# Kernel optimization log

Measured on AMD Instinct MI355X. Metric: run time of the kernel, lower is better.

## Reference

```python
import jax, jax.numpy as jnp
import numpy as np

B, C, H, W, D = 1, 128, 64, 64, 64
CQ = C // 8


def setup_inputs() -> dict:
    key = jax.random.key(0)
    ks = jax.random.split(key, 6)
    s = 0.05
    return {
        "x": jax.random.normal(ks[0], (B, C, H, W, D), jnp.float32),
        "y": jax.random.normal(ks[1], (B, C, H, W, D), jnp.float32),
        "Wq": jax.random.normal(ks[2], (CQ, C), jnp.float32) * s,
        "bq": jnp.zeros((CQ,), jnp.float32),
        "Wk": jax.random.normal(ks[3], (CQ, C), jnp.float32) * s,
        "bk": jnp.zeros((CQ,), jnp.float32),
        "Wv": jax.random.normal(ks[4], (C, C), jnp.float32) * s,
        "bv": jnp.zeros((C,), jnp.float32),
        # torch inits gamma to 0 (kills all attention grads); use a nonzero value
        "gamma": jax.random.normal(ks[5], (1,), jnp.float32),
    }


def _conv1x1(x, Wt, b):
    # 1x1x1 Conv3d == per-voxel linear over channels
    return jnp.einsum('bchwd,oc->bohwd', x, Wt) + b[None, :, None, None, None]


def _criss_cross(x, y, Wq, bq, Wk, bk, Wv, bv, gamma):
    Bs, Cs, Hs, Ws, Ds = x.shape
    Cq = Wq.shape[0]
    q = _conv1x1(x, Wq, bq)  # [B,Cq,H,W,D]
    k = _conv1x1(y, Wk, bk)  # [B,Cq,H,W,D]
    v = _conv1x1(x, Wv, bv)  # [B,C ,H,W,D]

    # exact transliteration of the torch permute/contiguous/view sequence
    qH = q.transpose(0, 3, 4, 1, 2).reshape(Bs * Ws * Ds, Cq, Hs).transpose(0, 2, 1)
    qW = q.transpose(0, 2, 4, 1, 3).reshape(Bs * Hs * Ds, Cq, Ws).transpose(0, 2, 1)
    qD = q.transpose(0, 2, 3, 1, 4).reshape(Bs * Hs * Ws, Cq, Ds).transpose(0, 2, 1)
    kH = k.transpose(0, 3, 4, 1, 2).reshape(Bs * Ws * Ds, Cq, Hs)
    kW = k.transpose(0, 2, 4, 1, 3).reshape(Bs * Hs * Ds, Cq, Ws)
    kD = k.transpose(0, 2, 3, 1, 4).reshape(Bs * Hs * Ws, Cq, Ds)
    vH = v.transpose(0, 3, 4, 1, 2).reshape(Bs * Ws * Ds, Cs, Hs)
    vW = v.transpose(0, 2, 4, 1, 3).reshape(Bs * Hs * Ds, Cs, Ws)
    vD = v.transpose(0, 2, 3, 1, 4).reshape(Bs * Hs * Ws, Cs, Ds)

    # INF(): -inf on the HxH diagonal, broadcast over the B*W*D batch
    inf_mask = jnp.where(jnp.eye(Hs, dtype=bool), -jnp.inf, 0.0)[None].astype(x.dtype)

    energy_H = (jnp.matmul(qH, kH) + inf_mask).reshape(Bs, Ws, Hs, Ds, Hs).transpose(0, 2, 1, 3, 4)
    energy_W = jnp.matmul(qW, kW).reshape(Bs, Hs, Ws, Ds, Ws)
    energy_D = jnp.matmul(qD, kD).reshape(Bs, Hs, Ws, Ds, Ds)

    # NOTE: original uses Softmax(dim=3) on the 5D concat -> softmax over the D axis
    concate = jax.nn.softmax(jnp.concatenate([energy_H, energy_W, energy_D], axis=4), axis=3)

    att_H = concate[..., 0:Hs].transpose(0, 2, 1, 3, 4).reshape(Bs * Ws * Ds, Hs, Hs)
    att_W = concate[..., Hs:Hs + Ws].reshape(Bs * Hs * Ds, Ws, Ws)
    att_D = concate[..., Hs + Ws:Hs + Ws + Ds].reshape(Bs * Hs * Ws, Ds, Ds)

    out_H = jnp.matmul(vH, att_H.transpose(0, 2, 1)).reshape(Bs, Ws, Cs, Hs, Ds).transpose(0, 2, 3, 1, 4)
    out_W = jnp.matmul(vW, att_W.transpose(0, 2, 1)).reshape(Bs, Hs, Cs, Ws, Ds).transpose(0, 2, 1, 3, 4)
    out_D = jnp.matmul(vD, att_D.transpose(0, 2, 1)).reshape(Bs, Hs, Cs, Ws, Ds).transpose(0, 2, 1, 3, 4)

    return gamma[0] * (out_H + out_W + out_D) + x


def reference(x, y, Wq, bq, Wk, bk, Wv, bv, gamma):
    return _criss_cross(x, y, Wq, bq, Wk, bk, Wv, bv, gamma)
```

## Files before the change

### kernel.cpp

```cpp
#include <hip/hip_runtime.h>

#define HWD 262144
#define WD  4096

typedef unsigned short bf16_t;
typedef unsigned short u16;
struct __align__(8) us4 { unsigned short x, y, z, w; };

typedef __bf16 bf16x8 __attribute__((ext_vector_type(8)));
typedef float  f32x4  __attribute__((ext_vector_type(4)));

__device__ inline float b2f(unsigned short u) {
    return __uint_as_float(((unsigned int)u) << 16);
}
__device__ inline unsigned short f2b(float f) {
    unsigned int u = __float_as_uint(f);
    u += 0x7fff + ((u >> 16) & 1);
    return (unsigned short)(u >> 16);
}

union FragU { us4 h[2]; bf16x8 v; };
__device__ inline bf16x8 ld8_a8(const u16* p) {
    FragU f; f.h[0] = *(const us4*)p; f.h[1] = *(const us4*)(p + 4); return f.v;
}
__device__ inline bf16x8 ld8_a16(const u16* p) {
    return *(const bf16x8*)p;
}

struct HL { bf16x8 h, l; };
__device__ inline HL split8(const float* w8) {
    FragU H, L;
    unsigned short hh[8], ll[8];
#pragma unroll
    for (int t = 0; t < 8; ++t) {
        hh[t] = f2b(w8[t]);
        ll[t] = f2b(w8[t] - b2f(hh[t]));
    }
    H.h[0].x = hh[0]; H.h[0].y = hh[1]; H.h[0].z = hh[2]; H.h[0].w = hh[3];
    H.h[1].x = hh[4]; H.h[1].y = hh[5]; H.h[1].z = hh[6]; H.h[1].w = hh[7];
    L.h[0].x = ll[0]; L.h[0].y = ll[1]; L.h[0].z = ll[2]; L.h[0].w = ll[3];
    L.h[1].x = ll[4]; L.h[1].y = ll[5]; L.h[1].z = ll[6]; L.h[1].w = ll[7];
    HL r; r.h = H.v; r.l = L.v; return r;
}

__global__ void prep_w_kernel(
    const float* __restrict__ Wv, const float* __restrict__ Wq,
    const float* __restrict__ Wk,
    u16* __restrict__ WSv, u16* __restrict__ WSq, u16* __restrict__ WSk)
{
    const int t = threadIdx.x;
    const float* W; u16* D; int m, ks;
    if (t < 512)      { W = Wv; D = WSv; m = t >> 2;          ks = t & 3; }
    else if (t < 576) { W = Wq; D = WSq; m = (t - 512) >> 2;  ks = t & 3; }
    else if (t < 640) { W = Wk; D = WSk; m = (t - 576) >> 2;  ks = t & 3; }
    else return;
#pragma unroll
    for (int j = 0; j < 32; ++j) {
        const float w = W[m * 128 + ks * 32 + j];
        const u16 h = f2b(w);
        const u16 l = f2b(w - b2f(h));
        D[((m * 4 + ks) * 2 + 0) * 32 + j] = h;
        D[((m * 4 + ks) * 2 + 1) * 32 + j] = l;
    }
}

__global__ __launch_bounds__(512, 4) void conv_x_mfma(
    const float* __restrict__ x, const u16* __restrict__ WSv,
    const u16* __restrict__ WSq,
    const float* __restrict__ bv, const float* __restrict__ bq,
    bf16_t* __restrict__ v, bf16_t* __restrict__ q)
{
    __shared__ __align__(16) u16 Xh[64][136];
    __shared__ __align__(16) u16 Xl[64][136];
    const int tid  = threadIdx.x;
    const int lane = tid & 63;
    const int wv   = tid >> 6;
    const int lg = lane >> 4, lr = lane & 15;
    const int n0 = blockIdx.x * 64;
    const int m0 = wv * 16;

    float v8[2][8];
#pragma unroll
    for (int gi = 0; gi < 2; ++gi) {
        const int g = wv + gi * 8;
#pragma unroll
        for (int s = 0; s < 8; ++s)
            v8[gi][s] = x[(size_t)(g * 8 + s) * HWD + n0 + lane];
    }

    bf16x8 Ah[4], Al[4], Qh[4], Ql[4];
#pragma unroll
    for (int ks = 0; ks < 4; ++ks) {
        Ah[ks] = ld8_a16(&WSv[(((m0 + lr) * 4 + ks) * 2 + 0) * 32 + lg * 8]);
        Al[ks] = ld8_a16(&WSv[(((m0 + lr) * 4 + ks) * 2 + 1) * 32 + lg * 8]);
    }
    if (wv < 4) {
#pragma unroll
        for (int ks = 0; ks < 4; ++ks) {
            Qh[ks] = ld8_a16(&WSq[((lr * 4 + ks) * 2 + 0) * 32 + lg * 8]);
            Ql[ks] = ld8_a16(&WSq[((lr * 4 + ks) * 2 + 1) * 32 + lg * 8]);
        }
    }

#pragma unroll
    for (int gi = 0; gi < 2; ++gi) {
        const int g = wv + gi * 8;
        HL hl = split8(v8[gi]);
        *(bf16x8*)&Xh[lane][g * 8] = hl.h;
        *(bf16x8*)&Xl[lane][g * 8] = hl.l;
    }
    __syncthreads();

    f32x4 acc[4];
#pragma unroll
    for (int ns = 0; ns < 4; ++ns) acc[ns] = (f32x4){0.f, 0.f, 0.f, 0.f};
    f32x4 accq = (f32x4){0.f, 0.f, 0.f, 0.f};
#pragma unroll
    for (int ks = 0; ks < 4; ++ks) {
#pragma unroll
        for (int ns = 0; ns < 4; ++ns) {
            const bf16x8 Bh = ld8_a16(&Xh[ns * 16 + lr][ks * 32 + lg * 8]);
            const bf16x8 Bl = ld8_a16(&Xl[ns * 16 + lr][ks * 32 + lg * 8]);
            acc[ns] = __builtin_amdgcn_mfma_f32_16x16x32_bf16(Ah[ks], Bh, acc[ns], 0, 0, 0);
            acc[ns] = __builtin_amdgcn_mfma_f32_16x16x32_bf16(Ah[ks], Bl, acc[ns], 0, 0, 0);
            acc[ns] = __builtin_amdgcn_mfma_f32_16x16x32_bf16(Al[ks], Bh, acc[ns], 0, 0, 0);
            if (wv < 4 && ns == wv) {
                accq = __builtin_amdgcn_mfma_f32_16x16x32_bf16(Qh[ks], Bh, accq, 0, 0, 0);
                accq = __builtin_amdgcn_mfma_f32_16x16x32_bf16(Qh[ks], Bl, accq, 0, 0, 0);
                accq = __builtin_amdgcn_mfma_f32_16x16x32_bf16(Ql[ks], Bh, accq, 0, 0, 0);
            }
        }
    }
#pragma unroll
    for (int ns = 0; ns < 4; ++ns)
#pragma unroll
        for (int r = 0; r < 4; ++r) {
            const int m = m0 + 4 * lg + r;
            v[(size_t)m * HWD + n0 + ns * 16 + lr] = f2b(acc[ns][r] + bv[m]);
        }
    if (wv < 4) {
#pragma unroll
        for (int r = 0; r < 4; ++r) {
            const int m = 4 * lg + r;
            q[(size_t)m * HWD + n0 + wv * 16 + lr] = f2b(accq[r] + bq[m]);
        }
    }
}

__global__ __launch_bounds__(256, 4) void conv_y_mfma(
    const float* __restrict__ y, const u16* __restrict__ WSk,
    const float* __restrict__ bk, bf16_t* __restrict__ k)
{
    __shared__ __align__(16) u16 Yh[64][136];
    __shared__ __align__(16) u16 Yl[64][136];
    const int tid  = threadIdx.x;
    const int lane = tid & 63;
    const int wv   = tid >> 6;
    const int lg = lane >> 4, lr = lane & 15;
    const int n0 = blockIdx.x * 64;
    const int n  = tid & 63;

    float v8[4][8];
#pragma unroll
    for (int gi = 0; gi < 4; ++gi) {
        const int g = (tid >> 6) * 4 + gi;
#pragma unroll
        for (int s = 0; s < 8; ++s)
            v8[gi][s] = y[(size_t)(g * 8 + s) * HWD + n0 + n];
    }

    bf16x8 Ah[4], Al[4];
#pragma unroll
    for (int ks = 0; ks < 4; ++ks) {
        Ah[ks] = ld8_a16(&WSk[((lr * 4 + ks) * 2 + 0) * 32 + lg * 8]);
        Al[ks] = ld8_a16(&WSk[((lr * 4 + ks) * 2 + 1) * 32 + lg * 8]);
    }

#pragma unroll
    for (int gi = 0; gi < 4; ++gi) {
        const int g = (tid >> 6) * 4 + gi;
        HL hl = split8(v8[gi]);
        *(bf16x8*)&Yh[n][g * 8] = hl.h;
        *(bf16x8*)&Yl[n][g * 8] = hl.l;
    }
    __syncthreads();

    f32x4 acc = (f32x4){0.f, 0.f, 0.f, 0.f};
#pragma unroll
    for (int ks = 0; ks < 4; ++ks) {
        const bf16x8 Bh = ld8_a16(&Yh[wv * 16 + lr][ks * 32 + lg * 8]);
        const bf16x8 Bl = ld8_a16(&Yl[wv * 16 + lr][ks * 32 + lg * 8]);
        acc = __builtin_amdgcn_mfma_f32_16x16x32_bf16(Ah[ks], Bh, acc, 0, 0, 0);
        acc = __builtin_amdgcn_mfma_f32_16x16x32_bf16(Ah[ks], Bl, acc, 0, 0, 0);
        acc = __builtin_amdgcn_mfma_f32_16x16x32_bf16(Al[ks], Bh, acc, 0, 0, 0);
    }
#pragma unroll
    for (int r = 0; r < 4; ++r) {
        const int m = 4 * lg + r;
        k[(size_t)m * HWD + n0 + wv * 16 + lr] = f2b(acc[r] + bk[m]);
    }
}

__global__ __launch_bounds__(256) void t_wd_kernel(
    const bf16_t* __restrict__ src, bf16_t* __restrict__ dst)
{
    const int h = blockIdx.x, c = blockIdx.y;
    __shared__ bf16_t tile[64][72];
    const size_t base = (size_t)c * HWD + h * WD;
    const int tid = threadIdx.x;
#pragma unroll
    for (int i = 0; i < 4; ++i) {
        const int f = (tid + i * 256) * 4;
        const int w = f >> 6, d = f & 63;
        const us4 val = *(const us4*)&src[base + w * 64 + d];
        tile[w][d] = val.x; tile[w][d + 1] = val.y;
        tile[w][d + 2] = val.z; tile[w][d + 3] = val.w;
    }
    __syncthreads();
#pragma unroll
    for (int i = 0; i < 4; ++i) {
        const int f = (tid + i * 256) * 4;
        const int d = f >> 6, w0 = f & 63;
        us4 o; o.x = tile[w0][d]; o.y = tile[w0 + 1][d];
        o.z = tile[w0 + 2][d]; o.w = tile[w0 + 3][d];
        *(us4*)&dst[base + d * 64 + w0] = o;
    }
}

__global__ __launch_bounds__(256) void t_hd_kernel(
    const bf16_t* __restrict__ src, bf16_t* __restrict__ dst)
{
    const int w = blockIdx.x, c = blockIdx.y;
    __shared__ bf16_t tile[64][72];
    const size_t cb = (size_t)c * HWD;
    const int tid = threadIdx.x;
#pragma unroll
    for (int i = 0; i < 4; ++i) {
        const int f = (tid + i * 256) * 4;
        const int h = f >> 6, d0 = f & 63;
        const us4 val = *(const us4*)&src[cb + h * WD + w * 64 + d0];
        tile[h][d0] = val.x; tile[h][d0 + 1] = val.y;
        tile[h][d0 + 2] = val.z; tile[h][d0 + 3] = val.w;
    }
    __syncthreads();
#pragma unroll
    for (int i = 0; i < 4; ++i) {
        const int f = (tid + i * 256) * 4;
        const int d = f >> 6, h0 = f & 63;
        us4 o; o.x = tile[h0][d]; o.y = tile[h0 + 1][d];
        o.z = tile[h0 + 2][d]; o.w = tile[h0 + 3][d];
        *(us4*)&dst[cb + w * WD + d * 64 + h0] = o;
    }
}

template<bool MASK>
__device__ __forceinline__ void cc_phase(
    const u16* __restrict__ qp, const u16* __restrict__ kp,
    const u16* __restrict__ vp, const size_t base, const int tid,
    u16 (*Qt)[36], u16 (*Kt)[36], u16 (*Vs)[72], u16 (*PB)[72], f32x4* acc)
{
    const int w  = tid >> 6;
    const int l  = tid & 63;
    const int lg = l >> 4, lr = l & 15;

    __syncthreads();
    const int c0 = (tid >> 6) * 4;
    const size_t gb = base + (tid & 63);
    us4 qv, kv;
    qv.x = qp[(size_t)(c0 + 0) * HWD + gb];
    qv.y = qp[(size_t)(c0 + 1) * HWD + gb];
    qv.z = qp[(size_t)(c0 + 2) * HWD + gb];
    qv.w = qp[(size_t)(c0 + 3) * HWD + gb];
    kv.x = kp[(size_t)(c0 + 0) * HWD + gb];
    kv.y = kp[(size_t)(c0 + 1) * HWD + gb];
    kv.z = kp[(size_t)(c0 + 2) * HWD + gb];
    kv.w = kp[(size_t)(c0 + 3) * HWD + gb];
    us4 vreg[8];
#pragma unroll
    for (int i = 0; i < 8; ++i) {
        const int f = (tid + i * 256) * 4;
        vreg[i] = *(const us4*)&vp[(size_t)(f >> 6) * HWD + base + (f & 63)];
    }
    {
        const int j = tid & 63;
        *(us4*)&Qt[j][c0] = qv;
        *(us4*)&Kt[j][c0] = kv;
        us4 z; z.x = z.y = z.z = z.w = 0;
        *(us4*)&Qt[j][16 + c0] = z;
        *(us4*)&Kt[j][16 + c0] = z;
    }
    __syncthreads();
    float pv[16];
    {
        const bf16x8 bk = ld8_a8(&Kt[16 * w + lr][8 * lg]);
#pragma unroll
        for (int ti = 0; ti < 4; ++ti) {
            const bf16x8 aq = ld8_a8(&Qt[16 * ti + lr][8 * lg]);
            f32x4 e = {0.f, 0.f, 0.f, 0.f};
            e = __builtin_amdgcn_mfma_f32_16x16x32_bf16(aq, bk, e, 0, 0, 0);
#pragma unroll
            for (int r = 0; r < 4; ++r) {
                float vv = e[r];
                if (MASK && (16 * ti + 4 * lg + r) == (16 * w + lr)) vv = -1e30f;
                pv[ti * 4 + r] = vv;
            }
        }
    }
    __syncthreads();
    {
        float m = -1e30f;
#pragma unroll
        for (int t = 0; t < 16; ++t) m = fmaxf(m, pv[t]);
        m = fmaxf(m, __shfl_xor(m, 16));
        m = fmaxf(m, __shfl_xor(m, 32));
        float ss = 0.f;
#pragma unroll
        for (int t = 0; t < 16; ++t) { pv[t] = __expf(pv[t] - m); ss += pv[t]; }
        ss += __shfl_xor(ss, 16);
        ss += __shfl_xor(ss, 32);
        const float inv = 1.f / ss;
        const int j = 16 * w + lr;
#pragma unroll
        for (int ti = 0; ti < 4; ++ti)
#pragma unroll
            for (int r = 0; r < 4; ++r)
                PB[16 * ti + 4 * lg + r][j] = f2b(pv[ti * 4 + r] * inv);
    }
#pragma unroll
    for (int i = 0; i < 8; ++i) {
        const int f = (tid + i * 256) * 4;
        *(us4*)&Vs[f >> 6][f & 63] = vreg[i];
    }
    __syncthreads();
#pragma unroll
    for (int ks = 0; ks < 2; ++ks) {
        const bf16x8 bp = ld8_a16(&PB[16 * w + lr][32 * ks + 8 * lg]);
#pragma unroll
        for (int tm = 0; tm < 8; ++tm) {
            const bf16x8 av = ld8_a16(&Vs[16 * tm + lr][32 * ks + 8 * lg]);
            acc[tm] = __builtin_amdgcn_mfma_f32_16x16x32_bf16(av, bp, acc[tm], 0, 0, 0);
        }
    }
}

__global__ __launch_bounds__(256, 4) void cc_wd_kernel(
    const bf16_t* __restrict__ q,  const bf16_t* __restrict__ k,
    const bf16_t* __restrict__ v,
    const bf16_t* __restrict__ qT, const bf16_t* __restrict__ kT,
    const bf16_t* __restrict__ vT,
    const float* __restrict__ x, const float* __restrict__ gamma,
    float* __restrict__ out)
{
    const int s   = blockIdx.x;
    const int hh  = blockIdx.y;
    const int tid = threadIdx.x;
    __shared__ __align__(16) u16 VsU[128][72];
    __shared__ __align__(16) u16 PB[64][72];
    u16 (*Qt)[36] = (u16(*)[36])&VsU[0][0];
    u16 (*Kt)[36] = (u16(*)[36])((u16*)&VsU[0][0] + 64 * 36);
    u16 (*Vs)[72] = VsU;
    f32x4 acc[8];
#pragma unroll
    for (int i = 0; i < 8; ++i) acc[i] = (f32x4){0.f, 0.f, 0.f, 0.f};

    const size_t base = (size_t)hh * WD + s * 64;
    for (int phase = 0; phase < 2; ++phase) {
        const u16* qp = phase ? q : qT;
        const u16* kp = phase ? k : kT;
        const u16* vp = phase ? v : vT;
        cc_phase<false>(qp, kp, vp, base, tid, Qt, Kt, Vs, PB, acc);
    }

    const int w = tid >> 6, l = tid & 63, lg = l >> 4, lr = l & 15;
    const int dd = 16 * w + lr;
    const float g = gamma[0];
#pragma unroll
    for (int tm = 0; tm < 8; ++tm)
#pragma unroll
        for (int r = 0; r < 4; ++r) {
            const int c = 16 * tm + 4 * lg + r;
            const size_t o = (size_t)(2 * s + (c >> 6)) * HWD +
                             (size_t)hh * WD + (size_t)(c & 63) * 64 + dd;
            out[o] = g * acc[tm][r] + x[o];
        }
}

__global__ __launch_bounds__(256, 4) void cc_h_kernel(
    const bf16_t* __restrict__ qH, const bf16_t* __restrict__ kH,
    const bf16_t* __restrict__ vH,
    const float* __restrict__ gamma, float* __restrict__ out)
{
    const int t   = blockIdx.x;
    const int ww  = blockIdx.y;
    const int tid = threadIdx.x;
    __shared__ __align__(16) u16 VsU[128][72];
    __shared__ __align__(16) u16 PB[64][72];
    u16 (*Qt)[36] = (u16(*)[36])&VsU[0][0];
    u16 (*Kt)[36] = (u16(*)[36])((u16*)&VsU[0][0] + 64 * 36);
    u16 (*Vs)[72] = VsU;
    f32x4 acc[8];
#pragma unroll
    for (int i = 0; i < 8; ++i) acc[i] = (f32x4){0.f, 0.f, 0.f, 0.f};

    const size_t base = (size_t)ww * WD + t * 64;
    cc_phase<true>(qH, kH, vH, base, tid, Qt, Kt, Vs, PB, acc);

    const int w = tid >> 6, l = tid & 63, lg = l >> 4, lr = l & 15;
    const int dd = 16 * w + lr;
    const float g = gamma[0];
#pragma unroll
    for (int tm = 0; tm < 8; ++tm)
#pragma unroll
        for (int r = 0; r < 4; ++r) {
            const int c = 16 * tm + 4 * lg + r;
            const size_t o = (size_t)(2 * t + (c >> 6)) * HWD +
                             (size_t)(c & 63) * WD + (size_t)ww * 64 + dd;
            out[o] += g * acc[tm][r];
        }
}

extern "C" void kernel_launch(void* const* d_in, const int* in_sizes, int n_in,
                              void* d_out, int out_size, void* d_ws, size_t ws_size,
                              hipStream_t stream)
{
    const float* x     = (const float*)d_in[0];
    const float* y     = (const float*)d_in[1];
    const float* Wq    = (const float*)d_in[2];
    const float* bq    = (const float*)d_in[3];
    const float* Wk    = (const float*)d_in[4];
    const float* bk    = (const float*)d_in[5];
    const float* Wv    = (const float*)d_in[6];
    const float* bv    = (const float*)d_in[7];
    const float* gamma = (const float*)d_in[8];
    float* out = (float*)d_out;

    bf16_t* A0 = (bf16_t*)d_ws;
    bf16_t* v  = A0;
    bf16_t* q  = A0 + (size_t)128 * HWD;
    bf16_t* k  = A0 + (size_t)144 * HWD;
    bf16_t* A1 = A0 + (size_t)160 * HWD;
    bf16_t* A2 = A1 + (size_t)160 * HWD;
    u16* WSv = (u16*)A1;
    u16* WSq = WSv + 32768;
    u16* WSk = WSq + 4096;

    prep_w_kernel<<<1, 640, 0, stream>>>(Wv, Wq, Wk, WSv, WSq, WSk);
    conv_x_mfma <<<4096, 512, 0, stream>>>(x, WSv, WSq, bv, bq, v, q);
    conv_y_mfma <<<4096, 256, 0, stream>>>(y, WSk, bk, k);
    t_wd_kernel <<<dim3(64, 160), 256, 0, stream>>>(A0, A1);
    t_hd_kernel <<<dim3(64, 160), 256, 0, stream>>>(A0, A2);
    cc_wd_kernel<<<dim3(64, 64), 256, 0, stream>>>(
        q, k, v, A1 + (size_t)128 * HWD, A1 + (size_t)144 * HWD, A1, x, gamma, out);
    cc_h_kernel <<<dim3(64, 64), 256, 0, stream>>>(
        A2 + (size_t)128 * HWD, A2 + (size_t)144 * HWD, A2, gamma, out);
}
```

Before: 567.9 us.

## Make conv kernels persistent over four tiles with register double-buffered loads

Each block of the conv_x and conv_y projection kernels now processes four 64-voxel tiles instead of one, and the grid shrinks by the same factor. The global loads for the next tile are issued into a second register buffer before the current tile is split, staged and multiplied, so load latency overlaps with MFMA work. The weight-fragment loads are also amortised over four tiles. In exchange the doubled load buffers raise register pressure, which may lower occupancy, and each tile needs an extra barrier.

```diff
diff --git a/kernel.cpp b/kernel.cpp
--- a/kernel.cpp
+++ b/kernel.cpp
@@ -76,17 +76,20 @@
     const int lane = tid & 63;
     const int wv   = tid >> 6;
     const int lg = lane >> 4, lr = lane & 15;
-    const int n0 = blockIdx.x * 64;
+    const int nb = blockIdx.x * 256;
     const int m0 = wv * 16;
 
-    float v8[2][8];
-#pragma unroll
-    for (int gi = 0; gi < 2; ++gi) {
-        const int g = wv + gi * 8;
-#pragma unroll
-        for (int s = 0; s < 8; ++s)
-            v8[gi][s] = x[(size_t)(g * 8 + s) * HWD + n0 + lane];
-    }
+    auto issue = [&](float (*dst)[8], int n0) {
+#pragma unroll
+        for (int gi = 0; gi < 2; ++gi) {
+            const int g = wv + gi * 8;
+#pragma unroll
+            for (int s = 0; s < 8; ++s)
+                dst[gi][s] = x[(size_t)(g * 8 + s) * HWD + n0 + lane];
+        }
+    };
+    float B0[2][8], B1[2][8];
+    issue(B0, nb);
 
     bf16x8 Ah[4], Al[4], Qh[4], Ql[4];
 #pragma unroll
@@ -103,47 +106,56 @@
     }
 
 #pragma unroll
-    for (int gi = 0; gi < 2; ++gi) {
-        const int g = wv + gi * 8;
-        HL hl = split8(v8[gi]);
-        *(bf16x8*)&Xh[lane][g * 8] = hl.h;
-        *(bf16x8*)&Xl[lane][g * 8] = hl.l;
-    }
-    __syncthreads();
-
-    f32x4 acc[4];
-#pragma unroll
-    for (int ns = 0; ns < 4; ++ns) acc[ns] = (f32x4){0.f, 0.f, 0.f, 0.f};
-    f32x4 accq = (f32x4){0.f, 0.f, 0.f, 0.f};
-#pragma unroll
-    for (int ks = 0; ks < 4; ++ks) {
-#pragma unroll
-        for (int ns = 0; ns < 4; ++ns) {
-            const bf16x8 Bh = ld8_a16(&Xh[ns * 16 + lr][ks * 32 + lg * 8]);
-            const bf16x8 Bl = ld8_a16(&Xl[ns * 16 + lr][ks * 32 + lg * 8]);
-            acc[ns] = __builtin_amdgcn_mfma_f32_16x16x32_bf16(Ah[ks], Bh, acc[ns], 0, 0, 0);
-            acc[ns] = __builtin_amdgcn_mfma_f32_16x16x32_bf16(Ah[ks], Bl, acc[ns], 0, 0, 0);
-            acc[ns] = __builtin_amdgcn_mfma_f32_16x16x32_bf16(Al[ks], Bh, acc[ns], 0, 0, 0);
-            if (wv < 4 && ns == wv) {
-                accq = __builtin_amdgcn_mfma_f32_16x16x32_bf16(Qh[ks], Bh, accq, 0, 0, 0);
-                accq = __builtin_amdgcn_mfma_f32_16x16x32_bf16(Qh[ks], Bl, accq, 0, 0, 0);
-                accq = __builtin_amdgcn_mfma_f32_16x16x32_bf16(Ql[ks], Bh, accq, 0, 0, 0);
+    for (int t = 0; t < 4; ++t) {
+        float (*cur)[8] = (t & 1) ? B1 : B0;
+        float (*nxt)[8] = (t & 1) ? B0 : B1;
+        const int n0 = nb + t * 64;
+        if (t < 3) issue(nxt, n0 + 64);
+
+#pragma unroll
+        for (int gi = 0; gi < 2; ++gi) {
+            const int g = wv + gi * 8;
+            HL hl = split8(cur[gi]);
+            *(bf16x8*)&Xh[lane][g * 8] = hl.h;
+            *(bf16x8*)&Xl[lane][g * 8] = hl.l;
+        }
+        __syncthreads();
+
+        f32x4 acc[4];
+#pragma unroll
+        for (int ns = 0; ns < 4; ++ns) acc[ns] = (f32x4){0.f, 0.f, 0.f, 0.f};
+        f32x4 accq = (f32x4){0.f, 0.f, 0.f, 0.f};
+#pragma unroll
+        for (int ks = 0; ks < 4; ++ks) {
+#pragma unroll
+            for (int ns = 0; ns < 4; ++ns) {
+                const bf16x8 Bh = ld8_a16(&Xh[ns * 16 + lr][ks * 32 + lg * 8]);
+                const bf16x8 Bl = ld8_a16(&Xl[ns * 16 + lr][ks * 32 + lg * 8]);
+                acc[ns] = __builtin_amdgcn_mfma_f32_16x16x32_bf16(Ah[ks], Bh, acc[ns], 0, 0, 0);
+                acc[ns] = __builtin_amdgcn_mfma_f32_16x16x32_bf16(Ah[ks], Bl, acc[ns], 0, 0, 0);
+                acc[ns] = __builtin_amdgcn_mfma_f32_16x16x32_bf16(Al[ks], Bh, acc[ns], 0, 0, 0);
+                if (wv < 4 && ns == wv) {
+                    accq = __builtin_amdgcn_mfma_f32_16x16x32_bf16(Qh[ks], Bh, accq, 0, 0, 0);
+                    accq = __builtin_amdgcn_mfma_f32_16x16x32_bf16(Qh[ks], Bl, accq, 0, 0, 0);
+                    accq = __builtin_amdgcn_mfma_f32_16x16x32_bf16(Ql[ks], Bh, accq, 0, 0, 0);
+                }
             }
         }
-    }
-#pragma unroll
-    for (int ns = 0; ns < 4; ++ns)
-#pragma unroll
-        for (int r = 0; r < 4; ++r) {
-            const int m = m0 + 4 * lg + r;
-            v[(size_t)m * HWD + n0 + ns * 16 + lr] = f2b(acc[ns][r] + bv[m]);
-        }
-    if (wv < 4) {
-#pragma unroll
-        for (int r = 0; r < 4; ++r) {
-            const int m = 4 * lg + r;
-            q[(size_t)m * HWD + n0 + wv * 16 + lr] = f2b(accq[r] + bq[m]);
-        }
+#pragma unroll
+        for (int ns = 0; ns < 4; ++ns)
+#pragma unroll
+            for (int r = 0; r < 4; ++r) {
+                const int m = m0 + 4 * lg + r;
+                v[(size_t)m * HWD + n0 + ns * 16 + lr] = f2b(acc[ns][r] + bv[m]);
+            }
+        if (wv < 4) {
+#pragma unroll
+            for (int r = 0; r < 4; ++r) {
+                const int m = 4 * lg + r;
+                q[(size_t)m * HWD + n0 + wv * 16 + lr] = f2b(accq[r] + bq[m]);
+            }
+        }
+        __syncthreads();
     }
 }
 
@@ -157,17 +169,20 @@
     const int lane = tid & 63;
     const int wv   = tid >> 6;
     const int lg = lane >> 4, lr = lane & 15;
-    const int n0 = blockIdx.x * 64;
+    const int nb = blockIdx.x * 256;
     const int n  = tid & 63;
 
-    float v8[4][8];
-#pragma unroll
-    for (int gi = 0; gi < 4; ++gi) {
-        const int g = (tid >> 6) * 4 + gi;
-#pragma unroll
-        for (int s = 0; s < 8; ++s)
-            v8[gi][s] = y[(size_t)(g * 8 + s) * HWD + n0 + n];
-    }
+    auto issue = [&](float (*dst)[8], int n0) {
+#pragma unroll
+        for (int gi = 0; gi < 4; ++gi) {
+            const int g = (tid >> 6) * 4 + gi;
+#pragma unroll
+            for (int s = 0; s < 8; ++s)
+                dst[gi][s] = y[(size_t)(g * 8 + s) * HWD + n0 + n];
+        }
+    };
+    float B0[4][8], B1[4][8];
+    issue(B0, nb);
 
     bf16x8 Ah[4], Al[4];
 #pragma unroll
@@ -177,27 +192,36 @@
     }
 
 #pragma unroll
-    for (int gi = 0; gi < 4; ++gi) {
-        const int g = (tid >> 6) * 4 + gi;
-        HL hl = split8(v8[gi]);
-        *(bf16x8*)&Yh[n][g * 8] = hl.h;
-        *(bf16x8*)&Yl[n][g * 8] = hl.l;
-    }
-    __syncthreads();
-
-    f32x4 acc = (f32x4){0.f, 0.f, 0.f, 0.f};
-#pragma unroll
-    for (int ks = 0; ks < 4; ++ks) {
-        const bf16x8 Bh = ld8_a16(&Yh[wv * 16 + lr][ks * 32 + lg * 8]);
-        const bf16x8 Bl = ld8_a16(&Yl[wv * 16 + lr][ks * 32 + lg * 8]);
-        acc = __builtin_amdgcn_mfma_f32_16x16x32_bf16(Ah[ks], Bh, acc, 0, 0, 0);
-        acc = __builtin_amdgcn_mfma_f32_16x16x32_bf16(Ah[ks], Bl, acc, 0, 0, 0);
-        acc = __builtin_amdgcn_mfma_f32_16x16x32_bf16(Al[ks], Bh, acc, 0, 0, 0);
-    }
-#pragma unroll
-    for (int r = 0; r < 4; ++r) {
-        const int m = 4 * lg + r;
-        k[(size_t)m * HWD + n0 + wv * 16 + lr] = f2b(acc[r] + bk[m]);
+    for (int t = 0; t < 4; ++t) {
+        float (*cur)[8] = (t & 1) ? B1 : B0;
+        float (*nxt)[8] = (t & 1) ? B0 : B1;
+        const int n0 = nb + t * 64;
+        if (t < 3) issue(nxt, n0 + 64);
+
+#pragma unroll
+        for (int gi = 0; gi < 4; ++gi) {
+            const int g = (tid >> 6) * 4 + gi;
+            HL hl = split8(cur[gi]);
+            *(bf16x8*)&Yh[n][g * 8] = hl.h;
+            *(bf16x8*)&Yl[n][g * 8] = hl.l;
+        }
+        __syncthreads();
+
+        f32x4 acc = (f32x4){0.f, 0.f, 0.f, 0.f};
+#pragma unroll
+        for (int ks = 0; ks < 4; ++ks) {
+            const bf16x8 Bh = ld8_a16(&Yh[wv * 16 + lr][ks * 32 + lg * 8]);
+            const bf16x8 Bl = ld8_a16(&Yl[wv * 16 + lr][ks * 32 + lg * 8]);
+            acc = __builtin_amdgcn_mfma_f32_16x16x32_bf16(Ah[ks], Bh, acc, 0, 0, 0);
+            acc = __builtin_amdgcn_mfma_f32_16x16x32_bf16(Ah[ks], Bl, acc, 0, 0, 0);
+            acc = __builtin_amdgcn_mfma_f32_16x16x32_bf16(Al[ks], Bh, acc, 0, 0, 0);
+        }
+#pragma unroll
+        for (int r = 0; r < 4; ++r) {
+            const int m = 4 * lg + r;
+            k[(size_t)m * HWD + n0 + wv * 16 + lr] = f2b(acc[r] + bk[m]);
+        }
+        __syncthreads();
     }
 }
 
@@ -445,8 +469,8 @@
     u16* WSk = WSq + 4096;
 
     prep_w_kernel<<<1, 640, 0, stream>>>(Wv, Wq, Wk, WSv, WSq, WSk);
-    conv_x_mfma <<<4096, 512, 0, stream>>>(x, WSv, WSq, bv, bq, v, q);
-    conv_y_mfma <<<4096, 256, 0, stream>>>(y, WSk, bk, k);
+    conv_x_mfma <<<1024, 512, 0, stream>>>(x, WSv, WSq, bv, bq, v, q);
+    conv_y_mfma <<<1024, 256, 0, stream>>>(y, WSk, bk, k);
     t_wd_kernel <<<dim3(64, 160), 256, 0, stream>>>(A0, A1);
     t_hd_kernel <<<dim3(64, 160), 256, 0, stream>>>(A0, A2);
     cc_wd_kernel<<<dim3(64, 64), 256, 0, stream>>>(
```

Result: slower. 640.0 us (+12.7%).
